# Optimization experiments

Hardware: AMD Instinct MI355X
Metric: run time of the kernel (lower is better)

The kernel has to match this reference:

```python
import jax, jax.numpy as jnp
import numpy as np

GROUPS = 8   # GroupNorm groups used by create_pat_conv*_blocks(..., groups=8)
EPS = 1e-5
K = 20       # num_neighbor


def group_norm(x, gamma, beta):
    # x: [B, C, ...spatial]
    B, C = x.shape[0], x.shape[1]
    shape = x.shape
    xg = x.reshape(B, GROUPS, C // GROUPS, -1)
    m = xg.mean(axis=(2, 3), keepdims=True)
    v = ((xg - m) ** 2).mean(axis=(2, 3), keepdims=True)
    xg = (xg - m) * jax.lax.rsqrt(v + EPS)
    x = xg.reshape(shape)
    bshape = (1, C) + (1,) * (len(shape) - 2)
    return x * gamma.reshape(bshape) + beta.reshape(bshape)


def conv_block(x, w, b, gamma, beta):
    # pointwise (kernel-size 1) conv + GroupNorm + ELU, works for 1d and 2d spatial
    y = jnp.einsum('oc,bc...->bo...', w, x) + b.reshape((1, -1) + (1,) * (x.ndim - 2))
    return jax.nn.elu(group_norm(y, gamma, beta))


def knn_graph(points, k):
    # points: [B, 3, N] -> neighbor coords [B, 3, N, k] (self included, dilation=1)
    sq = jnp.sum(points * points, axis=1)                      # [B, N]
    inner = jnp.einsum('bci,bcj->bij', points, points)         # [B, N, N]
    dist = sq[:, :, None] + sq[:, None, :] - 2.0 * inner       # squared pairwise dist
    _, idx = jax.lax.top_k(-dist, k)                           # [B, N, k] smallest dists
    neighbors = jnp.take_along_axis(points[:, :, None, :], idx[:, None, :, :], axis=3)
    return neighbors                                           # [B, 3, N, k]


def setup_inputs() -> dict:
    key = jax.random.key(0)
    B, N = 4, 8192
    dims1 = [6, 32, 64]
    dims2 = [64, 512, 1024]
    keys = iter(jax.random.split(key, 32))
    inp = {"points": jax.random.normal(next(keys), (B, 3, N), dtype=jnp.float32)}
    for tag, dims in (("p1", dims1), ("p2", dims2)):
        for i in range(len(dims) - 1):
            cin, cout = dims[i], dims[i + 1]
            inp[f"{tag}_w{i}"] = jax.random.normal(next(keys), (cout, cin), dtype=jnp.float32) / np.float32(np.sqrt(cin))
            inp[f"{tag}_b{i}"] = jnp.zeros((cout,), dtype=jnp.float32)
            inp[f"{tag}_g{i}"] = jnp.ones((cout,), dtype=jnp.float32)
            inp[f"{tag}_beta{i}"] = jnp.zeros((cout,), dtype=jnp.float32)
    return inp


def reference(points, p1_w0, p1_b0, p1_g0, p1_beta0, p1_w1, p1_b1, p1_g1, p1_beta1,
              p2_w0, p2_b0, p2_g0, p2_beta0, p2_w1, p2_b1, p2_g1, p2_beta1):
    neighbors = knn_graph(points, K)                             # [B, 3, N, K]
    center = jnp.broadcast_to(points[:, :, :, None], neighbors.shape)
    x = jnp.concatenate([center, neighbors - center], axis=1)   # [B, 6, N, K]
    x = conv_block(x, p1_w0, p1_b0, p1_g0, p1_beta0)            # [B, 32, N, K]
    x = conv_block(x, p1_w1, p1_b1, p1_g1, p1_beta1)            # [B, 64, N, K]
    x = jnp.max(x, axis=2)                                      # [B, 64, K] (faithful to source: max over dim=2)
    x = conv_block(x, p2_w0, p2_b0, p2_g0, p2_beta0)            # [B, 512, K]
    x = conv_block(x, p2_w1, p2_b1, p2_g1, p2_beta1)            # [B, 1024, K]
    return x
```

## Files before the change

### kernel.cpp

```cpp
#include <hip/hip_runtime.h>
#include <math.h>

#define NPTS   8192
#define BATCH  4
#define KNN    20
#define NKTOT  (NPTS*KNN)
#define EPS    1e-5f
#define TILE4  2048
#define QCAP   40

typedef float v2f __attribute__((ext_vector_type(2)));

__device__ __forceinline__ float elu(float x) { return x > 0.0f ? x : expm1f(x); }
__device__ __forceinline__ float eluf(float x) { return x > 0.0f ? x : __expf(x) - 1.0f; }
__device__ __forceinline__ v2f splat2(float x) { v2f v; v.x = x; v.y = x; return v; }
__device__ __forceinline__ float rfl(float x) {
    return __uint_as_float(__builtin_amdgcn_readfirstlane(__float_as_uint(x)));
}

__device__ __forceinline__ unsigned fenc(float f) {
    unsigned b = __float_as_uint(f);
    return b ^ ((unsigned)(((int)b) >> 31) | 0x80000000u);
}
__device__ __forceinline__ float fdec(unsigned u) {
    unsigned b = (u & 0x80000000u) ? (u ^ 0x80000000u) : ~u;
    return __uint_as_float(b);
}

__global__ __launch_bounds__(256) void prep_kernel(const float* __restrict__ points,
                                                   float4* __restrict__ pts4)
{
    const int t = blockIdx.x * 256 + threadIdx.x;
    const int b = t >> 13, n = t & (NPTS - 1);
    const float* px = points + b * 3 * NPTS;
    float x = px[n], y = px[NPTS + n], z = px[2 * NPTS + n];
    pts4[t] = make_float4(x, y, z, -0.5f * (x * x + y * y + z * z));
}

__global__ __launch_bounds__(512, 6) void knn_kernel(const float4* __restrict__ pts4,
                                                     int* __restrict__ idx_out)
{
    __shared__ float tx[TILE4], ty[TILE4], tz[TILE4], tw[TILE4];
    __shared__ unsigned long long queue[64][QCAP];
    __shared__ int qcnt[64];

    const int tid  = threadIdx.x;
    const int lane = tid & 63;
    const int wv   = tid >> 6;
    const int b    = blockIdx.x >> 7;
    const int q0   = (blockIdx.x & 127) * 64 + wv * 8;
    const float4* pb = pts4 + b * NPTS;

    if (tid < 64) qcnt[tid] = 0;

    float qx[8], qy[8], qz[8];
    v2f smax2[8];
#pragma unroll
    for (int q = 0; q < 8; ++q) {
        float4 qp = pb[q0 + q];
        qx[q] = rfl(qp.x); qy[q] = rfl(qp.y); qz[q] = rfl(qp.z);
        smax2[q] = splat2(-INFINITY);
    }

    float4 pf[4];
#pragma unroll
    for (int r = 0; r < 4; ++r) pf[r] = pb[tid + r * 512];

    for (int t = 0; t < NPTS / TILE4; ++t) {
        __syncthreads();
#pragma unroll
        for (int r = 0; r < 4; ++r) {
            int i = tid + r * 512;
            tx[i] = pf[r].x; ty[i] = pf[r].y; tz[i] = pf[r].z; tw[i] = pf[r].w;
        }
        __syncthreads();
        if (t + 1 < NPTS / TILE4) {
#pragma unroll
            for (int r = 0; r < 4; ++r) pf[r] = pb[(t + 1) * TILE4 + tid + r * 512];
        }
#pragma unroll 2
        for (int s = 0; s < TILE4 / 128; ++s) {
            v2f px = *(const v2f*)&tx[s * 128 + 2 * lane];
            v2f py = *(const v2f*)&ty[s * 128 + 2 * lane];
            v2f pz = *(const v2f*)&tz[s * 128 + 2 * lane];
            v2f pw = *(const v2f*)&tw[s * 128 + 2 * lane];
#pragma unroll
            for (int q = 0; q < 8; ++q) {
                v2f sv = __builtin_elementwise_fma(splat2(qx[q]), px,
                         __builtin_elementwise_fma(splat2(qy[q]), py,
                         __builtin_elementwise_fma(splat2(qz[q]), pz, pw)));
                smax2[q] = __builtin_elementwise_max(smax2[q], sv);
            }
        }
    }

#pragma unroll
    for (int r = 0; r < 4; ++r) pf[r] = pb[tid + r * 512];

    float sgate[8];
#pragma unroll
    for (int q = 0; q < 8; ++q) {
        float v = fmaxf(smax2[q].x, smax2[q].y);
#pragma unroll
        for (int k = 2; k <= 64; k <<= 1)
#pragma unroll
            for (int j = k >> 1; j >= 1; j >>= 1) {
                float o = __shfl_xor(v, j);
                bool up = ((lane & k) == 0);
                bool keepmin = (((lane & j) == 0) == up);
                v = keepmin ? fminf(v, o) : fmaxf(v, o);
            }
        float m = __shfl(v, 44);
        sgate[q] = m - 1e-4f - 1e-5f * fabsf(m);
    }

    for (int t = 0; t < NPTS / TILE4; ++t) {
        __syncthreads();
#pragma unroll
        for (int r = 0; r < 4; ++r) {
            int i = tid + r * 512;
            tx[i] = pf[r].x; ty[i] = pf[r].y; tz[i] = pf[r].z; tw[i] = pf[r].w;
        }
        __syncthreads();
        if (t + 1 < NPTS / TILE4) {
#pragma unroll
            for (int r = 0; r < 4; ++r) pf[r] = pb[(t + 1) * TILE4 + tid + r * 512];
        }
        for (int s = 0; s < TILE4 / 128; ++s) {
            v2f px = *(const v2f*)&tx[s * 128 + 2 * lane];
            v2f py = *(const v2f*)&ty[s * 128 + 2 * lane];
            v2f pz = *(const v2f*)&tz[s * 128 + 2 * lane];
            v2f pw = *(const v2f*)&tw[s * 128 + 2 * lane];
            const int jb = t * TILE4 + s * 128 + 2 * lane;
#pragma unroll
            for (int q = 0; q < 8; ++q) {
                v2f sv = __builtin_elementwise_fma(splat2(qx[q]), px,
                         __builtin_elementwise_fma(splat2(qy[q]), py,
                         __builtin_elementwise_fma(splat2(qz[q]), pz, pw)));
                if (fmaxf(sv.x, sv.y) >= sgate[q]) {
#pragma unroll
                    for (int h = 0; h < 2; ++h) {
                        float svh = h ? sv.y : sv.x;
                        if (svh >= sgate[q]) {
                            int slot = atomicAdd(&qcnt[wv * 8 + q], 1);
                            if (slot < QCAP) {
                                unsigned long long key =
                                    ((unsigned long long)fenc(svh) << 32)
                                    | (unsigned)(NPTS - 1 - (jb + h));
                                queue[wv * 8 + q][slot] = key;
                            }
                        }
                    }
                }
            }
        }
    }
    __syncthreads();

#pragma unroll
    for (int q = 0; q < 8; ++q) {
        int cq = qcnt[wv * 8 + q]; cq = cq < QCAP ? cq : QCAP;
        unsigned long long key = (lane < cq) ? queue[wv * 8 + q][lane] : 0ull;
#pragma unroll
        for (int k = 2; k <= 64; k <<= 1)
#pragma unroll
            for (int j = k >> 1; j >= 1; j >>= 1) {
                unsigned long long o = __shfl_xor(key, j);
                bool up = ((lane & k) == 0);
                bool keepmax = (((lane & j) == 0) == up);
                bool omax = o > key;
                key = (keepmax == omax) ? o : key;
            }
        if (lane < KNN)
            idx_out[(b * NPTS + q0 + q) * KNN + lane] =
                NPTS - 1 - (int)(unsigned)(key & 0xFFFFFFFFu);
    }
}

__global__ __launch_bounds__(256) void moments_x_kernel(const float* __restrict__ points,
                                                        const int* __restrict__ idx,
                                                        float* __restrict__ sums1p)
{
    const int t = blockIdx.x * 256 + threadIdx.x;
    const int b = blockIdx.x / 640;
    const int r = t - b * NKTOT;
    const int n = r / KNN;
    const float* px = points + b * 3 * NPTS;
    const int j = idx[t];
    float cx = px[n], cy = px[NPTS + n], cz = px[2 * NPTS + n];
    float v[27];
    v[0] = cx; v[1] = cy; v[2] = cz;
    v[3] = px[j] - cx; v[4] = px[NPTS + j] - cy; v[5] = px[2 * NPTS + j] - cz;
    int p = 6;
#pragma unroll
    for (int d = 0; d < 6; ++d)
#pragma unroll
        for (int e = d; e < 6; ++e) v[p++] = v[d] * v[e];
#pragma unroll
    for (int i = 0; i < 27; ++i)
        for (int o = 32; o > 0; o >>= 1) v[i] += __shfl_xor(v[i], o);

    __shared__ float red[4][27];
    const int lane = threadIdx.x & 63, w = threadIdx.x >> 6;
    if (lane == 0)
#pragma unroll
        for (int i = 0; i < 27; ++i) red[w][i] = v[i];
    __syncthreads();
    if (threadIdx.x < 27) {
        float acc = red[0][threadIdx.x] + red[1][threadIdx.x] + red[2][threadIdx.x] + red[3][threadIdx.x];
        int slot = blockIdx.x & 63;
        atomicAdd(&sums1p[(slot * BATCH + b) * 27 + threadIdx.x], acc);
    }
}

__global__ void finalize1_kernel(const float* __restrict__ sums1p,
                                 const float* __restrict__ w1, const float* __restrict__ b1,
                                 const float* __restrict__ g1, const float* __restrict__ beta1,
                                 float* __restrict__ w1f)
{
    __shared__ float S[BATCH][27];
    const int t = threadIdx.x;
    if (t < 108) {
        int b = t / 27, i = t % 27;
        float acc = 0.f;
        for (int s = 0; s < 64; ++s) acc += sums1p[(s * BATCH + b) * 27 + i];
        S[b][i] = acc;
    }
    __syncthreads();
    const int b = t >> 5, c = t & 31;
    const float invS = 1.0f / (float)NKTOT;
    float Ex[6], M[6][6];
#pragma unroll
    for (int d = 0; d < 6; ++d) Ex[d] = S[b][d] * invS;
    int p = 6;
#pragma unroll
    for (int d = 0; d < 6; ++d)
#pragma unroll
        for (int e = d; e < 6; ++e) { float v = S[b][p++] * invS; M[d][e] = v; M[e][d] = v; }
    const int g = c >> 2;
    float msum = 0.f, qsum = 0.f;
    for (int cc = g * 4; cc < g * 4 + 4; ++cc) {
        float w[6];
#pragma unroll
        for (int d = 0; d < 6; ++d) w[d] = w1[cc * 6 + d];
        float dotEx = 0.f;
#pragma unroll
        for (int d = 0; d < 6; ++d) dotEx += w[d] * Ex[d];
        float Ey = dotEx + b1[cc];
        float Ey2 = 0.f;
#pragma unroll
        for (int d = 0; d < 6; ++d)
#pragma unroll
            for (int e = 0; e < 6; ++e) Ey2 += w[d] * w[e] * M[d][e];
        Ey2 += 2.0f * b1[cc] * dotEx + b1[cc] * b1[cc];
        msum += Ey; qsum += Ey2;
    }
    float m = msum * 0.25f;
    float var = qsum * 0.25f - m * m;
    float inv = rsqrtf(var + EPS);
    float s = g1[c] * inv;
    float tt = s * (b1[c] - m) + beta1[c];
    float* o = w1f + (b * 32 + c) * 8;
#pragma unroll
    for (int d = 0; d < 6; ++d) o[d] = s * w1[c * 6 + d];
    o[6] = tt; o[7] = 0.f;
}

__global__ __launch_bounds__(256, 5) void fused_main_kernel(
    const float4* __restrict__ pts4, const int* __restrict__ idxb,
    const float* __restrict__ w1f, const float* __restrict__ w2, const float* __restrict__ b2,
    float* __restrict__ sums2p, unsigned int* __restrict__ maxenc, unsigned int* __restrict__ minenc)
{
    __shared__ __align__(16) float w2t[32 * 64];
    __shared__ __align__(16) float z1s[32 * 128];
    __shared__ __align__(16) float4 w1s4[64];
    __shared__ float b2s[64];
    __shared__ float redmx[256], redmn[256], sqred[128];

    const int t   = threadIdx.x;
    const int blk = blockIdx.x;
    const int nc  = blk & 15;
    const int k   = (blk >> 4) % 20;
    const int b   = blk / 320;

    for (int i = t; i < 512; i += 256) {
        float4 v = ((const float4*)w2)[i];
        int c = i >> 3, kq = (i & 7) * 4;
        w2t[(kq + 0) * 64 + c] = v.x; w2t[(kq + 1) * 64 + c] = v.y;
        w2t[(kq + 2) * 64 + c] = v.z; w2t[(kq + 3) * 64 + c] = v.w;
    }
    if (t < 64) { w1s4[t] = ((const float4*)w1f)[b * 64 + t]; b2s[t] = b2[t]; }

    const int wvi  = t >> 6;
    const int nf   = t & 127;
    const int cgf  = t >> 7;
    const int cq   = t & 15;
    const int ng   = t >> 4;
    const int c0   = cq * 4;
    const int n0   = ng * 8;
    const float4* pb = pts4 + b * NPTS;
    const int nbase = nc * 512;

    float mx[4], mn[4];
#pragma unroll
    for (int ci = 0; ci < 4; ++ci) { mx[ci] = -INFINITY; mn[ci] = INFINITY; }
    float gs = 0.f, gq = 0.f;

    for (int ph = 0; ph < 4; ++ph) {
        const int n = nbase + ph * 128 + nf;
        const int j = idxb[(b * NPTS + n) * KNN + k];
        float4 c4 = pb[n];
        float4 e4 = pb[j];
        float x0[6] = { c4.x, c4.y, c4.z, e4.x - c4.x, e4.y - c4.y, e4.z - c4.z };

        __syncthreads();
#pragma unroll
        for (int jj = 0; jj < 16; ++jj) {
            int c = cgf * 16 + jj;
            float4 wA = w1s4[c * 2 + 0];
            float4 wB = w1s4[c * 2 + 1];
            float z = wB.z;
            z = fmaf(wA.x, x0[0], z); z = fmaf(wA.y, x0[1], z); z = fmaf(wA.z, x0[2], z);
            z = fmaf(wA.w, x0[3], z); z = fmaf(wB.x, x0[4], z); z = fmaf(wB.y, x0[5], z);
            z1s[c * 128 + nf] = eluf(z);
        }
        __syncthreads();

        float acc[4][8];
#pragma unroll
        for (int ci = 0; ci < 4; ++ci) {
            float bb = b2s[c0 + ci];
#pragma unroll
            for (int pj = 0; pj < 8; ++pj) acc[ci][pj] = bb;
        }
#pragma unroll
        for (int kk = 0; kk < 32; ++kk) {
            float4 av = *(const float4*)&w2t[kk * 64 + c0];
            float4 z0 = *(const float4*)&z1s[kk * 128 + n0];
            float4 z1v = *(const float4*)&z1s[kk * 128 + n0 + 4];
            float avv[4] = { av.x, av.y, av.z, av.w };
            float zvv[8] = { z0.x, z0.y, z0.z, z0.w, z1v.x, z1v.y, z1v.z, z1v.w };
#pragma unroll
            for (int ci = 0; ci < 4; ++ci)
#pragma unroll
                for (int pj = 0; pj < 8; ++pj) acc[ci][pj] = fmaf(avv[ci], zvv[pj], acc[ci][pj]);
        }
#pragma unroll
        for (int ci = 0; ci < 4; ++ci)
#pragma unroll
            for (int pj = 0; pj < 8; ++pj) {
                float v = acc[ci][pj];
                gs += v; gq = fmaf(v, v, gq);
                mx[ci] = fmaxf(mx[ci], v); mn[ci] = fminf(mn[ci], v);
            }
    }

#pragma unroll
    for (int m = 16; m <= 32; m <<= 1) {
#pragma unroll
        for (int ci = 0; ci < 4; ++ci) {
            mx[ci] = fmaxf(mx[ci], __shfl_xor(mx[ci], m));
            mn[ci] = fminf(mn[ci], __shfl_xor(mn[ci], m));
        }
        gs += __shfl_xor(gs, m);
        gq += __shfl_xor(gq, m);
    }
    if ((t & 63) < 16) {
#pragma unroll
        for (int ci = 0; ci < 4; ++ci) {
            redmx[wvi * 64 + cq * 4 + ci] = mx[ci];
            redmn[wvi * 64 + cq * 4 + ci] = mn[ci];
        }
        sqred[(wvi * 16 + cq) * 2 + 0] = gs;
        sqred[(wvi * 16 + cq) * 2 + 1] = gq;
    }
    __syncthreads();
    if (t < 64) {
        float m = fmaxf(fmaxf(redmx[t], redmx[64 + t]), fmaxf(redmx[128 + t], redmx[192 + t]));
        atomicMax(&maxenc[(b * 64 + t) * KNN + k], fenc(m));
    } else if (t < 128) {
        int c = t - 64;
        float m = fminf(fminf(redmn[c], redmn[64 + c]), fminf(redmn[128 + c], redmn[192 + c]));
        atomicMin(&minenc[(b * 64 + c) * KNN + k], fenc(m));
    } else if (t < 144) {
        int i2 = t - 128, g = i2 >> 1, w = i2 & 1;
        float v = 0.f;
#pragma unroll
        for (int wv2 = 0; wv2 < 4; ++wv2)
            v += sqred[(wv2 * 16 + 2 * g) * 2 + w] + sqred[(wv2 * 16 + 2 * g + 1) * 2 + w];
        int slot = blk & 63;
        atomicAdd(&sums2p[((slot * BATCH + b) * 8 + g) * 2 + w], v);
    }
}

__global__ void build_m1_kernel(const float* __restrict__ sums2p,
                                const unsigned int* __restrict__ maxenc,
                                const unsigned int* __restrict__ minenc,
                                const float* __restrict__ gamma, const float* __restrict__ beta,
                                float* __restrict__ m1)
{
    const int t = blockIdx.x * 256 + threadIdx.x;
    const int b = t / 1280;
    const int r = t - b * 1280;
    const int c = r / 20;
    const int g = c >> 3;
    float s = 0.f, q = 0.f;
    for (int sl = 0; sl < 64; ++sl) {
        s += sums2p[((sl * BATCH + b) * 8 + g) * 2 + 0];
        q += sums2p[((sl * BATCH + b) * 8 + g) * 2 + 1];
    }
    const float cnt = 8.0f * (float)NKTOT;
    float m = s / cnt;
    float var = q / cnt - m * m;
    float inv = rsqrtf(var + EPS);
    float sc = gamma[c] * inv;
    float tt = beta[c] - sc * m;
    float y = (sc >= 0.f) ? fdec(maxenc[t]) : fdec(minenc[t]);
    m1[t] = elu(sc * y + tt);
}

template <int CIN, int SLOTS>
__global__ void p2_gemm_kernel(const float* __restrict__ zin, const float* __restrict__ w,
                               const float* __restrict__ bias, float* __restrict__ yout,
                               float* __restrict__ sumsp, int chans_per_group)
{
    const int t = blockIdx.x * 256 + threadIdx.x;
    const int per_b = (gridDim.x * 256) / BATCH;
    const int b = t / per_b;
    const int r = t - b * per_b;
    const int o = r / 20;
    const int k = r - o * 20;
    const float* zb = zin + b * CIN * 20;
    const float* wrow = w + o * CIN;
    float acc = bias[o];
    for (int c = 0; c < CIN; c += 4) {
        float4 wv = *(const float4*)&wrow[c];
        acc += wv.x * zb[(c + 0) * 20 + k] + wv.y * zb[(c + 1) * 20 + k]
             + wv.z * zb[(c + 2) * 20 + k] + wv.w * zb[(c + 3) * 20 + k];
    }
    yout[t] = acc;

    __shared__ float ls[16];
    if (threadIdx.x < 16) ls[threadIdx.x] = 0.f;
    __syncthreads();
    const int g = o / chans_per_group;
    atomicAdd(&ls[g * 2 + 0], acc);
    atomicAdd(&ls[g * 2 + 1], acc * acc);
    __syncthreads();
    if (threadIdx.x < 16) {
        int slot = blockIdx.x & (SLOTS - 1);
        atomicAdd(&sumsp[(slot * BATCH + b) * 16 + threadIdx.x], ls[threadIdx.x]);
    }
}

template <int SLOTS>
__global__ void p2_finalize_kernel(const float* __restrict__ y, const float* __restrict__ sumsp,
                                   const float* __restrict__ gamma, const float* __restrict__ beta,
                                   float* __restrict__ z, int chans_per_group, float cnt)
{
    const int t = blockIdx.x * 256 + threadIdx.x;
    const int per_b = (gridDim.x * 256) / BATCH;
    const int b = t / per_b;
    const int r = t - b * per_b;
    const int o = r / 20;
    const int g = o / chans_per_group;
    float s = 0.f, q = 0.f;
    for (int sl = 0; sl < SLOTS; ++sl) {
        s += sumsp[(sl * BATCH + b) * 16 + g * 2 + 0];
        q += sumsp[(sl * BATCH + b) * 16 + g * 2 + 1];
    }
    float m = s / cnt;
    float var = q / cnt - m * m;
    float inv = rsqrtf(var + EPS);
    float v = gamma[o] * inv * (y[t] - m) + beta[o];
    z[t] = elu(v);
}

extern "C" void kernel_launch(void* const* d_in, const int* in_sizes, int n_in,
                              void* d_out, int out_size, void* d_ws, size_t ws_size,
                              hipStream_t stream)
{
    const float* points  = (const float*)d_in[0];
    const float* p1_w0   = (const float*)d_in[1];
    const float* p1_b0   = (const float*)d_in[2];
    const float* p1_g0   = (const float*)d_in[3];
    const float* p1_bt0  = (const float*)d_in[4];
    const float* p1_w1   = (const float*)d_in[5];
    const float* p1_b1   = (const float*)d_in[6];
    const float* p1_g1   = (const float*)d_in[7];
    const float* p1_bt1  = (const float*)d_in[8];
    const float* p2_w0   = (const float*)d_in[9];
    const float* p2_b0   = (const float*)d_in[10];
    const float* p2_g0   = (const float*)d_in[11];
    const float* p2_bt0  = (const float*)d_in[12];
    const float* p2_w1   = (const float*)d_in[13];
    const float* p2_b1   = (const float*)d_in[14];
    const float* p2_g1   = (const float*)d_in[15];
    const float* p2_bt1  = (const float*)d_in[16];
    float* out = (float*)d_out;

    float* ws = (float*)d_ws;
    int*      idx     = (int*)ws;
    float*    sums1p  = ws + 655360;
    float*    sums2p  = sums1p + 6912;
    float*    sumsAp  = sums2p + 4096;
    float*    sumsBp  = sumsAp + 1024;
    unsigned* maxenc  = (unsigned*)(sumsBp + 1024);
    unsigned* minenc  = maxenc + 5120;
    float*    w1f     = (float*)(minenc + 5120);
    float*    m1      = w1f + 1024;
    float*    yp2a    = m1 + 5120;
    float*    zp2a    = yp2a + 40960;
    float*    yp2b    = zp2a + 40960;
    float4*   pts4    = (float4*)yp2a;

    hipMemsetAsync(sums1p, 0, (6912 + 4096 + 1024 + 1024 + 5120) * sizeof(float), stream);
    hipMemsetAsync(minenc, 0xFF, 5120 * sizeof(unsigned), stream);

    prep_kernel<<<128, 256, 0, stream>>>(points, pts4);
    knn_kernel<<<512, 512, 0, stream>>>(pts4, idx);
    moments_x_kernel<<<2560, 256, 0, stream>>>(points, idx, sums1p);
    finalize1_kernel<<<1, 128, 0, stream>>>(sums1p, p1_w0, p1_b0, p1_g0, p1_bt0, w1f);
    fused_main_kernel<<<1280, 256, 0, stream>>>(pts4, idx, w1f, p1_w1, p1_b1,
                                                sums2p, maxenc, minenc);
    build_m1_kernel<<<20, 256, 0, stream>>>(sums2p, maxenc, minenc, p1_g1, p1_bt1, m1);
    p2_gemm_kernel<64, 16><<<160, 256, 0, stream>>>(m1, p2_w0, p2_b0, yp2a, sumsAp, 64);
    p2_finalize_kernel<16><<<160, 256, 0, stream>>>(yp2a, sumsAp, p2_g0, p2_bt0, zp2a, 64, 1280.0f);
    p2_gemm_kernel<512, 16><<<320, 256, 0, stream>>>(zp2a, p2_w1, p2_b1, yp2b, sumsBp, 128);
    p2_finalize_kernel<16><<<320, 256, 0, stream>>>(yp2b, sumsBp, p2_g1, p2_bt1, out, 128, 2560.0f);
}
```

Baseline: 286.3 us.

## Split kNN candidate scan across wave pairs and transpose neighbor index layout

Result: no change. 287.8 us (+0.5%).

```diff
diff --git a/kernel.cpp b/kernel.cpp
--- a/kernel.cpp
+++ b/kernel.cpp
@@ -6,8 +6,7 @@
 #define KNN    20
 #define NKTOT  (NPTS*KNN)
 #define EPS    1e-5f
-#define TILE4  2048
-#define QCAP   40
+#define QCAP   56
 
 typedef float v2f __attribute__((ext_vector_type(2)));
 
@@ -37,21 +36,24 @@
     pts4[t] = make_float4(x, y, z, -0.5f * (x * x + y * y + z * z));
 }
 
-__global__ __launch_bounds__(512, 6) void knn_kernel(const float4* __restrict__ pts4,
+__global__ __launch_bounds__(512, 8) void knn_kernel(const float4* __restrict__ pts4,
                                                      int* __restrict__ idx_out)
 {
-    __shared__ float tx[TILE4], ty[TILE4], tz[TILE4], tw[TILE4];
-    __shared__ unsigned long long queue[64][QCAP];
-    __shared__ int qcnt[64];
+    __shared__ unsigned long long queue[32][QCAP];
+    __shared__ int qcnt[32];
+    __shared__ float gsh[2][32];
 
     const int tid  = threadIdx.x;
     const int lane = tid & 63;
     const int wv   = tid >> 6;
-    const int b    = blockIdx.x >> 7;
-    const int q0   = (blockIdx.x & 127) * 64 + wv * 8;
+    const int oct  = wv >> 1;
+    const int par  = wv & 1;
+    const int b    = blockIdx.x >> 8;
+    const int q0   = (blockIdx.x & 255) * 32 + oct * 8;
     const float4* pb = pts4 + b * NPTS;
-
-    if (tid < 64) qcnt[tid] = 0;
+    const int cbase = par * (NPTS / 2);
+
+    if (tid < 32) qcnt[tid] = 0;
 
     float qx[8], qy[8], qz[8];
     v2f smax2[8];
@@ -62,42 +64,22 @@
         smax2[q] = splat2(-INFINITY);
     }
 
-    float4 pf[4];
-#pragma unroll
-    for (int r = 0; r < 4; ++r) pf[r] = pb[tid + r * 512];
-
-    for (int t = 0; t < NPTS / TILE4; ++t) {
-        __syncthreads();
-#pragma unroll
-        for (int r = 0; r < 4; ++r) {
-            int i = tid + r * 512;
-            tx[i] = pf[r].x; ty[i] = pf[r].y; tz[i] = pf[r].z; tw[i] = pf[r].w;
-        }
-        __syncthreads();
-        if (t + 1 < NPTS / TILE4) {
-#pragma unroll
-            for (int r = 0; r < 4; ++r) pf[r] = pb[(t + 1) * TILE4 + tid + r * 512];
-        }
-#pragma unroll 2
-        for (int s = 0; s < TILE4 / 128; ++s) {
-            v2f px = *(const v2f*)&tx[s * 128 + 2 * lane];
-            v2f py = *(const v2f*)&ty[s * 128 + 2 * lane];
-            v2f pz = *(const v2f*)&tz[s * 128 + 2 * lane];
-            v2f pw = *(const v2f*)&tw[s * 128 + 2 * lane];
-#pragma unroll
-            for (int q = 0; q < 8; ++q) {
-                v2f sv = __builtin_elementwise_fma(splat2(qx[q]), px,
-                         __builtin_elementwise_fma(splat2(qy[q]), py,
-                         __builtin_elementwise_fma(splat2(qz[q]), pz, pw)));
-                smax2[q] = __builtin_elementwise_max(smax2[q], sv);
-            }
-        }
-    }
-
-#pragma unroll
-    for (int r = 0; r < 4; ++r) pf[r] = pb[tid + r * 512];
-
-    float sgate[8];
+#pragma unroll 4
+    for (int t = 0; t < NPTS / 2 / 128; ++t) {
+        float4 p0 = pb[cbase + t * 128 + 2 * lane];
+        float4 p1 = pb[cbase + t * 128 + 2 * lane + 1];
+        v2f px = { p0.x, p1.x }, py = { p0.y, p1.y };
+        v2f pz = { p0.z, p1.z }, pw = { p0.w, p1.w };
+#pragma unroll
+        for (int q = 0; q < 8; ++q) {
+            v2f sv = __builtin_elementwise_fma(splat2(qx[q]), px,
+                     __builtin_elementwise_fma(splat2(qy[q]), py,
+                     __builtin_elementwise_fma(splat2(qz[q]), pz, pw)));
+            smax2[q] = __builtin_elementwise_max(smax2[q], sv);
+        }
+    }
+
+    float gloc[8];
 #pragma unroll
     for (int q = 0; q < 8; ++q) {
         float v = fmaxf(smax2[q].x, smax2[q].y);
@@ -110,45 +92,42 @@
                 bool keepmin = (((lane & j) == 0) == up);
                 v = keepmin ? fminf(v, o) : fmaxf(v, o);
             }
-        float m = __shfl(v, 44);
+        gloc[q] = __shfl(v, 44);
+    }
+    if (lane == 0) {
+#pragma unroll
+        for (int q = 0; q < 8; ++q) gsh[par][oct * 8 + q] = gloc[q];
+    }
+    __syncthreads();
+    float sgate[8];
+#pragma unroll
+    for (int q = 0; q < 8; ++q) {
+        float m = fmaxf(gsh[0][oct * 8 + q], gsh[1][oct * 8 + q]);
         sgate[q] = m - 1e-4f - 1e-5f * fabsf(m);
     }
 
-    for (int t = 0; t < NPTS / TILE4; ++t) {
-        __syncthreads();
-#pragma unroll
-        for (int r = 0; r < 4; ++r) {
-            int i = tid + r * 512;
-            tx[i] = pf[r].x; ty[i] = pf[r].y; tz[i] = pf[r].z; tw[i] = pf[r].w;
-        }
-        __syncthreads();
-        if (t + 1 < NPTS / TILE4) {
-#pragma unroll
-            for (int r = 0; r < 4; ++r) pf[r] = pb[(t + 1) * TILE4 + tid + r * 512];
-        }
-        for (int s = 0; s < TILE4 / 128; ++s) {
-            v2f px = *(const v2f*)&tx[s * 128 + 2 * lane];
-            v2f py = *(const v2f*)&ty[s * 128 + 2 * lane];
-            v2f pz = *(const v2f*)&tz[s * 128 + 2 * lane];
-            v2f pw = *(const v2f*)&tw[s * 128 + 2 * lane];
-            const int jb = t * TILE4 + s * 128 + 2 * lane;
-#pragma unroll
-            for (int q = 0; q < 8; ++q) {
-                v2f sv = __builtin_elementwise_fma(splat2(qx[q]), px,
-                         __builtin_elementwise_fma(splat2(qy[q]), py,
-                         __builtin_elementwise_fma(splat2(qz[q]), pz, pw)));
-                if (fmaxf(sv.x, sv.y) >= sgate[q]) {
-#pragma unroll
-                    for (int h = 0; h < 2; ++h) {
-                        float svh = h ? sv.y : sv.x;
-                        if (svh >= sgate[q]) {
-                            int slot = atomicAdd(&qcnt[wv * 8 + q], 1);
-                            if (slot < QCAP) {
-                                unsigned long long key =
-                                    ((unsigned long long)fenc(svh) << 32)
-                                    | (unsigned)(NPTS - 1 - (jb + h));
-                                queue[wv * 8 + q][slot] = key;
-                            }
+    for (int t = 0; t < NPTS / 2 / 128; ++t) {
+        float4 p0 = pb[cbase + t * 128 + 2 * lane];
+        float4 p1 = pb[cbase + t * 128 + 2 * lane + 1];
+        v2f px = { p0.x, p1.x }, py = { p0.y, p1.y };
+        v2f pz = { p0.z, p1.z }, pw = { p0.w, p1.w };
+        const int jb = cbase + t * 128 + 2 * lane;
+#pragma unroll
+        for (int q = 0; q < 8; ++q) {
+            v2f sv = __builtin_elementwise_fma(splat2(qx[q]), px,
+                     __builtin_elementwise_fma(splat2(qy[q]), py,
+                     __builtin_elementwise_fma(splat2(qz[q]), pz, pw)));
+            if (fmaxf(sv.x, sv.y) >= sgate[q]) {
+#pragma unroll
+                for (int h = 0; h < 2; ++h) {
+                    float svh = h ? sv.y : sv.x;
+                    if (svh >= sgate[q]) {
+                        int slot = atomicAdd(&qcnt[oct * 8 + q], 1);
+                        if (slot < QCAP) {
+                            unsigned long long key =
+                                ((unsigned long long)fenc(svh) << 32)
+                                | (unsigned)(NPTS - 1 - (jb + h));
+                            queue[oct * 8 + q][slot] = key;
                         }
                     }
                 }
@@ -158,9 +137,10 @@
     __syncthreads();
 
 #pragma unroll
-    for (int q = 0; q < 8; ++q) {
-        int cq = qcnt[wv * 8 + q]; cq = cq < QCAP ? cq : QCAP;
-        unsigned long long key = (lane < cq) ? queue[wv * 8 + q][lane] : 0ull;
+    for (int qq = 0; qq < 4; ++qq) {
+        const int q = par * 4 + qq;
+        int cq = qcnt[oct * 8 + q]; cq = cq < QCAP ? cq : QCAP;
+        unsigned long long key = (lane < cq) ? queue[oct * 8 + q][lane] : 0ull;
 #pragma unroll
         for (int k = 2; k <= 64; k <<= 1)
 #pragma unroll
@@ -172,7 +152,7 @@
                 key = (keepmax == omax) ? o : key;
             }
         if (lane < KNN)
-            idx_out[(b * NPTS + q0 + q) * KNN + lane] =
+            idx_out[(b * KNN + lane) * NPTS + (q0 + q)] =
                 NPTS - 1 - (int)(unsigned)(key & 0xFFFFFFFFu);
     }
 }
@@ -184,7 +164,7 @@
     const int t = blockIdx.x * 256 + threadIdx.x;
     const int b = blockIdx.x / 640;
     const int r = t - b * NKTOT;
-    const int n = r / KNN;
+    const int n = r & (NPTS - 1);
     const float* px = points + b * 3 * NPTS;
     const int j = idx[t];
     float cx = px[n], cy = px[NPTS + n], cz = px[2 * NPTS + n];
@@ -300,6 +280,7 @@
     const int n0   = ng * 8;
     const float4* pb = pts4 + b * NPTS;
     const int nbase = nc * 512;
+    const int* idxrow = idxb + (b * KNN + k) * NPTS;
 
     float mx[4], mn[4];
 #pragma unroll
@@ -308,7 +289,7 @@
 
     for (int ph = 0; ph < 4; ++ph) {
         const int n = nbase + ph * 128 + nf;
-        const int j = idxb[(b * NPTS + n) * KNN + k];
+        const int j = idxrow[n];
         float4 c4 = pb[n];
         float4 e4 = pb[j];
         float x0[6] = { c4.x, c4.y, c4.z, e4.x - c4.x, e4.y - c4.y, e4.z - c4.z };
@@ -518,7 +499,7 @@
     hipMemsetAsync(minenc, 0xFF, 5120 * sizeof(unsigned), stream);
 
     prep_kernel<<<128, 256, 0, stream>>>(points, pts4);
-    knn_kernel<<<512, 512, 0, stream>>>(pts4, idx);
+    knn_kernel<<<1024, 512, 0, stream>>>(pts4, idx);
     moments_x_kernel<<<2560, 256, 0, stream>>>(points, idx, sums1p);
     finalize1_kernel<<<1, 128, 0, stream>>>(sums1p, p1_w0, p1_b0, p1_g0, p1_bt0, w1f);
     fused_main_kernel<<<1280, 256, 0, stream>>>(pts4, idx, w1f, p1_w1, p1_b1,
```

## Fuse p2 stage into one kernel, transpose kNN index layout, batch moments

Applied to the files above, without the earlier changes.

Measured after the change: 352.7 us. 1.23x slower.

```diff
diff --git a/kernel.cpp b/kernel.cpp
--- a/kernel.cpp
+++ b/kernel.cpp
@@ -172,30 +172,39 @@
                 key = (keepmax == omax) ? o : key;
             }
         if (lane < KNN)
-            idx_out[(b * NPTS + q0 + q) * KNN + lane] =
+            idx_out[(b * KNN + lane) * NPTS + (q0 + q)] =
                 NPTS - 1 - (int)(unsigned)(key & 0xFFFFFFFFu);
     }
 }
 
-__global__ __launch_bounds__(256) void moments_x_kernel(const float* __restrict__ points,
+__global__ __launch_bounds__(256) void moments_x_kernel(const float4* __restrict__ pts4,
                                                         const int* __restrict__ idx,
                                                         float* __restrict__ sums1p)
 {
-    const int t = blockIdx.x * 256 + threadIdx.x;
-    const int b = blockIdx.x / 640;
-    const int r = t - b * NKTOT;
-    const int n = r / KNN;
-    const float* px = points + b * 3 * NPTS;
-    const int j = idx[t];
-    float cx = px[n], cy = px[NPTS + n], cz = px[2 * NPTS + n];
+    const int b  = blockIdx.x / 80;
+    const int r0 = (blockIdx.x - b * 80) * 2048;
+    const float4* pb = pts4 + b * NPTS;
+    const int* ib = idx + b * NKTOT;
+
     float v[27];
-    v[0] = cx; v[1] = cy; v[2] = cz;
-    v[3] = px[j] - cx; v[4] = px[NPTS + j] - cy; v[5] = px[2 * NPTS + j] - cz;
-    int p = 6;
-#pragma unroll
-    for (int d = 0; d < 6; ++d)
-#pragma unroll
-        for (int e = d; e < 6; ++e) v[p++] = v[d] * v[e];
+#pragma unroll
+    for (int i = 0; i < 27; ++i) v[i] = 0.f;
+
+    for (int e = 0; e < 8; ++e) {
+        const int id = r0 + e * 256 + threadIdx.x;
+        const int n = id & (NPTS - 1);
+        const int j = ib[id];
+        float4 c4 = pb[n];
+        float4 e4 = pb[j];
+        float x[6] = { c4.x, c4.y, c4.z, e4.x - c4.x, e4.y - c4.y, e4.z - c4.z };
+        int p = 6;
+#pragma unroll
+        for (int d = 0; d < 6; ++d) {
+            v[d] += x[d];
+#pragma unroll
+            for (int ee = d; ee < 6; ++ee) v[p++] += x[d] * x[ee];
+        }
+    }
 #pragma unroll
     for (int i = 0; i < 27; ++i)
         for (int o = 32; o > 0; o >>= 1) v[i] += __shfl_xor(v[i], o);
@@ -300,6 +309,7 @@
     const int n0   = ng * 8;
     const float4* pb = pts4 + b * NPTS;
     const int nbase = nc * 512;
+    const int* idxrow = idxb + (b * KNN + k) * NPTS;
 
     float mx[4], mn[4];
 #pragma unroll
@@ -308,7 +318,7 @@
 
     for (int ph = 0; ph < 4; ++ph) {
         const int n = nbase + ph * 128 + nf;
-        const int j = idxb[(b * NPTS + n) * KNN + k];
+        const int j = idxrow[n];
         float4 c4 = pb[n];
         float4 e4 = pb[j];
         float x0[6] = { c4.x, c4.y, c4.z, e4.x - c4.x, e4.y - c4.y, e4.z - c4.z };
@@ -393,87 +403,134 @@
     }
 }
 
-__global__ void build_m1_kernel(const float* __restrict__ sums2p,
-                                const unsigned int* __restrict__ maxenc,
-                                const unsigned int* __restrict__ minenc,
-                                const float* __restrict__ gamma, const float* __restrict__ beta,
-                                float* __restrict__ m1)
-{
-    const int t = blockIdx.x * 256 + threadIdx.x;
-    const int b = t / 1280;
-    const int r = t - b * 1280;
-    const int c = r / 20;
-    const int g = c >> 3;
-    float s = 0.f, q = 0.f;
-    for (int sl = 0; sl < 64; ++sl) {
-        s += sums2p[((sl * BATCH + b) * 8 + g) * 2 + 0];
-        q += sums2p[((sl * BATCH + b) * 8 + g) * 2 + 1];
-    }
-    const float cnt = 8.0f * (float)NKTOT;
-    float m = s / cnt;
-    float var = q / cnt - m * m;
-    float inv = rsqrtf(var + EPS);
-    float sc = gamma[c] * inv;
-    float tt = beta[c] - sc * m;
-    float y = (sc >= 0.f) ? fdec(maxenc[t]) : fdec(minenc[t]);
-    m1[t] = elu(sc * y + tt);
-}
-
-template <int CIN, int SLOTS>
-__global__ void p2_gemm_kernel(const float* __restrict__ zin, const float* __restrict__ w,
-                               const float* __restrict__ bias, float* __restrict__ yout,
-                               float* __restrict__ sumsp, int chans_per_group)
-{
-    const int t = blockIdx.x * 256 + threadIdx.x;
-    const int per_b = (gridDim.x * 256) / BATCH;
-    const int b = t / per_b;
-    const int r = t - b * per_b;
-    const int o = r / 20;
-    const int k = r - o * 20;
-    const float* zb = zin + b * CIN * 20;
-    const float* wrow = w + o * CIN;
-    float acc = bias[o];
-    for (int c = 0; c < CIN; c += 4) {
-        float4 wv = *(const float4*)&wrow[c];
-        acc += wv.x * zb[(c + 0) * 20 + k] + wv.y * zb[(c + 1) * 20 + k]
-             + wv.z * zb[(c + 2) * 20 + k] + wv.w * zb[(c + 3) * 20 + k];
-    }
-    yout[t] = acc;
-
-    __shared__ float ls[16];
-    if (threadIdx.x < 16) ls[threadIdx.x] = 0.f;
-    __syncthreads();
-    const int g = o / chans_per_group;
-    atomicAdd(&ls[g * 2 + 0], acc);
-    atomicAdd(&ls[g * 2 + 1], acc * acc);
-    __syncthreads();
-    if (threadIdx.x < 16) {
-        int slot = blockIdx.x & (SLOTS - 1);
-        atomicAdd(&sumsp[(slot * BATCH + b) * 16 + threadIdx.x], ls[threadIdx.x]);
-    }
-}
-
-template <int SLOTS>
-__global__ void p2_finalize_kernel(const float* __restrict__ y, const float* __restrict__ sumsp,
-                                   const float* __restrict__ gamma, const float* __restrict__ beta,
-                                   float* __restrict__ z, int chans_per_group, float cnt)
-{
-    const int t = blockIdx.x * 256 + threadIdx.x;
-    const int per_b = (gridDim.x * 256) / BATCH;
-    const int b = t / per_b;
-    const int r = t - b * per_b;
-    const int o = r / 20;
-    const int g = o / chans_per_group;
-    float s = 0.f, q = 0.f;
-    for (int sl = 0; sl < SLOTS; ++sl) {
-        s += sumsp[(sl * BATCH + b) * 16 + g * 2 + 0];
-        q += sumsp[(sl * BATCH + b) * 16 + g * 2 + 1];
-    }
-    float m = s / cnt;
-    float var = q / cnt - m * m;
-    float inv = rsqrtf(var + EPS);
-    float v = gamma[o] * inv * (y[t] - m) + beta[o];
-    z[t] = elu(v);
+__global__ __launch_bounds__(512) void p2_fused_kernel(
+    const float* __restrict__ sums2p,
+    const unsigned int* __restrict__ maxenc, const unsigned int* __restrict__ minenc,
+    const float* __restrict__ g1, const float* __restrict__ bt1,
+    const float* __restrict__ wA, const float* __restrict__ bA,
+    const float* __restrict__ gA, const float* __restrict__ btA,
+    const float* __restrict__ wB, const float* __restrict__ bB,
+    const float* __restrict__ gB, const float* __restrict__ btB,
+    float* __restrict__ out)
+{
+    __shared__ float m1s[64 * 20];
+    __shared__ float ya[512 * 20];
+    __shared__ float statsl[16];
+    __shared__ float m2mean[8], m2inv[8], meanA[8], invA[8], gnb[2];
+
+    const int t = threadIdx.x;
+    const int b = blockIdx.x >> 3;
+    const int g = blockIdx.x & 7;
+
+    if (t < 16) {
+        int gg = t >> 1, w = t & 1;
+        float s = 0.f;
+        for (int sl = 0; sl < 64; ++sl) s += sums2p[((sl * BATCH + b) * 8 + gg) * 2 + w];
+        statsl[t] = s;
+    }
+    __syncthreads();
+    if (t < 8) {
+        const float cnt = 8.0f * (float)NKTOT;
+        float m = statsl[t * 2 + 0] / cnt;
+        float var = statsl[t * 2 + 1] / cnt - m * m;
+        m2mean[t] = m; m2inv[t] = rsqrtf(var + EPS);
+    }
+    __syncthreads();
+    for (int i = t; i < 1280; i += 512) {
+        int c = i / 20;
+        int gg = c >> 3;
+        float sc = g1[c] * m2inv[gg];
+        float tt = bt1[c] - sc * m2mean[gg];
+        float y = (sc >= 0.f) ? fdec(maxenc[b * 1280 + i]) : fdec(minenc[b * 1280 + i]);
+        m1s[i] = elu(sc * y + tt);
+    }
+    __syncthreads();
+
+    float va[20];
+#pragma unroll
+    for (int r = 0; r < 20; ++r) {
+        int oid = r * 512 + t;
+        int o = oid / 20, k = oid - o * 20;
+        float acc = bA[o];
+        const float* wr = wA + o * 64;
+#pragma unroll
+        for (int c = 0; c < 64; c += 4) {
+            float4 wv = *(const float4*)&wr[c];
+            acc += wv.x * m1s[(c + 0) * 20 + k] + wv.y * m1s[(c + 1) * 20 + k]
+                 + wv.z * m1s[(c + 2) * 20 + k] + wv.w * m1s[(c + 3) * 20 + k];
+        }
+        va[r] = acc;
+        ya[o * 20 + k] = acc;
+    }
+    __syncthreads();
+
+    {
+        int team = t >> 6, lane = t & 63;
+        float s = 0.f, q = 0.f;
+        for (int i = lane; i < 1280; i += 64) {
+            float v = ya[team * 1280 + i];
+            s += v; q = fmaf(v, v, q);
+        }
+#pragma unroll
+        for (int m = 1; m <= 32; m <<= 1) { s += __shfl_xor(s, m); q += __shfl_xor(q, m); }
+        if (lane == 0) {
+            float mm = s / 1280.0f;
+            float var = q / 1280.0f - mm * mm;
+            meanA[team] = mm; invA[team] = rsqrtf(var + EPS);
+        }
+    }
+    __syncthreads();
+#pragma unroll
+    for (int r = 0; r < 20; ++r) {
+        int oid = r * 512 + t;
+        int o = oid / 20, k = oid - o * 20;
+        int gg = o >> 6;
+        ya[o * 20 + k] = elu(gA[o] * invA[gg] * (va[r] - meanA[gg]) + btA[o]);
+    }
+    __syncthreads();
+
+    float vb[5];
+#pragma unroll
+    for (int r = 0; r < 5; ++r) {
+        int oid = r * 512 + t;
+        int ol = oid / 20, k = oid - ol * 20;
+        int o = g * 128 + ol;
+        float acc = bB[o];
+        const float* wr = wB + o * 512;
+#pragma unroll 8
+        for (int c = 0; c < 512; c += 4) {
+            float4 wv = *(const float4*)&wr[c];
+            acc += wv.x * ya[(c + 0) * 20 + k] + wv.y * ya[(c + 1) * 20 + k]
+                 + wv.z * ya[(c + 2) * 20 + k] + wv.w * ya[(c + 3) * 20 + k];
+        }
+        vb[r] = acc;
+    }
+    {
+        float s = 0.f, q = 0.f;
+#pragma unroll
+        for (int r = 0; r < 5; ++r) { s += vb[r]; q = fmaf(vb[r], vb[r], q); }
+#pragma unroll
+        for (int m = 1; m <= 32; m <<= 1) { s += __shfl_xor(s, m); q += __shfl_xor(q, m); }
+        int wvid = t >> 6, lane = t & 63;
+        if (lane == 0) { statsl[wvid * 2] = s; statsl[wvid * 2 + 1] = q; }
+    }
+    __syncthreads();
+    if (t == 0) {
+        float s = 0.f, q = 0.f;
+        for (int w = 0; w < 8; ++w) { s += statsl[w * 2]; q += statsl[w * 2 + 1]; }
+        float mm = s / 2560.0f;
+        float var = q / 2560.0f - mm * mm;
+        gnb[0] = mm; gnb[1] = rsqrtf(var + EPS);
+    }
+    __syncthreads();
+    const float mB = gnb[0], iB = gnb[1];
+#pragma unroll
+    for (int r = 0; r < 5; ++r) {
+        int oid = r * 512 + t;
+        int ol = oid / 20, k = oid - ol * 20;
+        int o = g * 128 + ol;
+        out[b * 20480 + o * 20 + k] = elu(gB[o] * iB * (vb[r] - mB) + btB[o]);
+    }
 }
 
 extern "C" void kernel_launch(void* const* d_in, const int* in_sizes, int n_in,
@@ -503,29 +560,23 @@
     int*      idx     = (int*)ws;
     float*    sums1p  = ws + 655360;
     float*    sums2p  = sums1p + 6912;
-    float*    sumsAp  = sums2p + 4096;
-    float*    sumsBp  = sumsAp + 1024;
-    unsigned* maxenc  = (unsigned*)(sumsBp + 1024);
+    float*    pad0    = sums2p + 4096;
+    unsigned* maxenc  = (unsigned*)(pad0 + 2048);
     unsigned* minenc  = maxenc + 5120;
     float*    w1f     = (float*)(minenc + 5120);
-    float*    m1      = w1f + 1024;
-    float*    yp2a    = m1 + 5120;
-    float*    zp2a    = yp2a + 40960;
-    float*    yp2b    = zp2a + 40960;
-    float4*   pts4    = (float4*)yp2a;
-
-    hipMemsetAsync(sums1p, 0, (6912 + 4096 + 1024 + 1024 + 5120) * sizeof(float), stream);
+    float*    pts4f   = w1f + 1024;
+    float4*   pts4    = (float4*)pts4f;
+
+    hipMemsetAsync(sums1p, 0, (6912 + 4096 + 2048 + 5120) * sizeof(float), stream);
     hipMemsetAsync(minenc, 0xFF, 5120 * sizeof(unsigned), stream);
 
     prep_kernel<<<128, 256, 0, stream>>>(points, pts4);
     knn_kernel<<<512, 512, 0, stream>>>(pts4, idx);
-    moments_x_kernel<<<2560, 256, 0, stream>>>(points, idx, sums1p);
+    moments_x_kernel<<<320, 256, 0, stream>>>(pts4, idx, sums1p);
     finalize1_kernel<<<1, 128, 0, stream>>>(sums1p, p1_w0, p1_b0, p1_g0, p1_bt0, w1f);
     fused_main_kernel<<<1280, 256, 0, stream>>>(pts4, idx, w1f, p1_w1, p1_b1,
                                                 sums2p, maxenc, minenc);
-    build_m1_kernel<<<20, 256, 0, stream>>>(sums2p, maxenc, minenc, p1_g1, p1_bt1, m1);
-    p2_gemm_kernel<64, 16><<<160, 256, 0, stream>>>(m1, p2_w0, p2_b0, yp2a, sumsAp, 64);
-    p2_finalize_kernel<16><<<160, 256, 0, stream>>>(yp2a, sumsAp, p2_g0, p2_bt0, zp2a, 64, 1280.0f);
-    p2_gemm_kernel<512, 16><<<320, 256, 0, stream>>>(zp2a, p2_w1, p2_b1, yp2b, sumsBp, 128);
-    p2_finalize_kernel<16><<<320, 256, 0, stream>>>(yp2b, sumsBp, p2_g1, p2_bt1, out, 128, 2560.0f);
-}
+    p2_fused_kernel<<<32, 512, 0, stream>>>(sums2p, maxenc, minenc, p1_g1, p1_bt1,
+                                            p2_w0, p2_b0, p2_g0, p2_bt0,
+                                            p2_w1, p2_b1, p2_g1, p2_bt1, out);
+}
```

## Transpose kNN index layout to [B,K,N] and batch moments accumulation per thread

Applied to the files above, without the earlier changes.

Measured after the change: 272.8 us. -4.7%, faster.

```diff
diff --git a/kernel.cpp b/kernel.cpp
--- a/kernel.cpp
+++ b/kernel.cpp
@@ -172,30 +172,39 @@
                 key = (keepmax == omax) ? o : key;
             }
         if (lane < KNN)
-            idx_out[(b * NPTS + q0 + q) * KNN + lane] =
+            idx_out[(b * KNN + lane) * NPTS + (q0 + q)] =
                 NPTS - 1 - (int)(unsigned)(key & 0xFFFFFFFFu);
     }
 }
 
-__global__ __launch_bounds__(256) void moments_x_kernel(const float* __restrict__ points,
+__global__ __launch_bounds__(256) void moments_x_kernel(const float4* __restrict__ pts4,
                                                         const int* __restrict__ idx,
                                                         float* __restrict__ sums1p)
 {
-    const int t = blockIdx.x * 256 + threadIdx.x;
-    const int b = blockIdx.x / 640;
-    const int r = t - b * NKTOT;
-    const int n = r / KNN;
-    const float* px = points + b * 3 * NPTS;
-    const int j = idx[t];
-    float cx = px[n], cy = px[NPTS + n], cz = px[2 * NPTS + n];
+    const int b  = blockIdx.x / 80;
+    const int r0 = (blockIdx.x - b * 80) * 2048;
+    const float4* pb = pts4 + b * NPTS;
+    const int* ib = idx + b * NKTOT;
+
     float v[27];
-    v[0] = cx; v[1] = cy; v[2] = cz;
-    v[3] = px[j] - cx; v[4] = px[NPTS + j] - cy; v[5] = px[2 * NPTS + j] - cz;
-    int p = 6;
-#pragma unroll
-    for (int d = 0; d < 6; ++d)
-#pragma unroll
-        for (int e = d; e < 6; ++e) v[p++] = v[d] * v[e];
+#pragma unroll
+    for (int i = 0; i < 27; ++i) v[i] = 0.f;
+
+    for (int e = 0; e < 8; ++e) {
+        const int id = r0 + e * 256 + threadIdx.x;
+        const int n = id & (NPTS - 1);
+        const int j = ib[id];
+        float4 c4 = pb[n];
+        float4 e4 = pb[j];
+        float x[6] = { c4.x, c4.y, c4.z, e4.x - c4.x, e4.y - c4.y, e4.z - c4.z };
+        int p = 6;
+#pragma unroll
+        for (int d = 0; d < 6; ++d) {
+            v[d] += x[d];
+#pragma unroll
+            for (int ee = d; ee < 6; ++ee) v[p++] += x[d] * x[ee];
+        }
+    }
 #pragma unroll
     for (int i = 0; i < 27; ++i)
         for (int o = 32; o > 0; o >>= 1) v[i] += __shfl_xor(v[i], o);
@@ -300,6 +309,7 @@
     const int n0   = ng * 8;
     const float4* pb = pts4 + b * NPTS;
     const int nbase = nc * 512;
+    const int* idxrow = idxb + (b * KNN + k) * NPTS;
 
     float mx[4], mn[4];
 #pragma unroll
@@ -308,7 +318,7 @@
 
     for (int ph = 0; ph < 4; ++ph) {
         const int n = nbase + ph * 128 + nf;
-        const int j = idxb[(b * NPTS + n) * KNN + k];
+        const int j = idxrow[n];
         float4 c4 = pb[n];
         float4 e4 = pb[j];
         float x0[6] = { c4.x, c4.y, c4.z, e4.x - c4.x, e4.y - c4.y, e4.z - c4.z };
@@ -519,7 +529,7 @@
 
     prep_kernel<<<128, 256, 0, stream>>>(points, pts4);
     knn_kernel<<<512, 512, 0, stream>>>(pts4, idx);
-    moments_x_kernel<<<2560, 256, 0, stream>>>(points, idx, sums1p);
+    moments_x_kernel<<<320, 256, 0, stream>>>(pts4, idx, sums1p);
     finalize1_kernel<<<1, 128, 0, stream>>>(sums1p, p1_w0, p1_b0, p1_g0, p1_bt0, w1f);
     fused_main_kernel<<<1280, 256, 0, stream>>>(pts4, idx, w1f, p1_w1, p1_b1,
                                                 sums2p, maxenc, minenc);
```
